# Kernel tuning notes

Measured on AMD Instinct MI355X. Metric: run time of the kernel, lower is better.

The kernel has to match this reference:

```python
import jax, jax.numpy as jnp
import numpy as np

N_NODES = 50000
N_EDGES = 800000
FEAT = 128


def setup_inputs() -> dict:
    key = jax.random.key(0)
    k1, k2, k3, k4 = jax.random.split(key, 4)
    x = jax.random.normal(k1, (N_NODES, FEAT), dtype=jnp.float32)
    a = jax.random.normal(k2, (FEAT, 1), dtype=jnp.float32) * (1.414 / np.sqrt(FEAT))
    row = jax.random.randint(k3, (N_EDGES,), 0, N_NODES, dtype=jnp.int64)
    col = jax.random.randint(k4, (N_EDGES,), 0, N_NODES, dtype=jnp.int64)
    return {"x": x, "a": a, "row": row, "col": col}


def reference(x, a, row, col):
    n = x.shape[0]
    # per-node score e = x @ a, squeezed to [N]
    e = jnp.squeeze(x @ a, axis=-1)
    # gather per-edge score from the destination (column) node, as in e[col]
    vals = e[col]                                            # [E]
    # sparse row-wise softmax (numerically stable via segment max)
    m = jax.ops.segment_max(vals, row, num_segments=n)       # [N]
    m = jnp.where(jnp.isfinite(m), m, 0.0)                   # empty rows -> 0
    ex = jnp.exp(vals - m[row])                              # [E]
    denom = jax.ops.segment_sum(ex, row, num_segments=n)     # [N]
    att = ex / denom[row]                                    # [E]
    # sparse-dense matmul: h[i] = sum_j att_ij * x[j]
    h_prime = jax.ops.segment_sum(att[:, None] * x[col], row, num_segments=n)
    return h_prime
```

## Files before the change

### kernel.cpp

```cpp
#include <hip/hip_runtime.h>
#include <hip/hip_bf16.h>
#include <math.h>

#define FEAT 128

__device__ __forceinline__ int pack_bf162(float lo, float hi) {
    __hip_bfloat162 b = __float22bfloat162_rn(make_float2(lo, hi));
    union { __hip_bfloat162 b; int i; } u;
    u.b = b;
    return u.i;
}

__device__ __forceinline__ float2 bf2_to_f2(int b) {
    union { int i; __hip_bfloat162 b; } u;
    u.i = b;
    return __bfloat1622float2(u.b);
}

__device__ __forceinline__ void fma8(float* acc, int4 v, float w) {
    float2 f0 = bf2_to_f2(v.x), f1 = bf2_to_f2(v.y);
    float2 f2 = bf2_to_f2(v.z), f3 = bf2_to_f2(v.w);
    acc[0] += w * f0.x; acc[1] += w * f0.y;
    acc[2] += w * f1.x; acc[3] += w * f1.y;
    acc[4] += w * f2.x; acc[5] += w * f2.y;
    acc[6] += w * f3.x; acc[7] += w * f3.y;
}

__global__ void dot_hist_kernel(const float* __restrict__ x, const float* __restrict__ a,
                                const int* __restrict__ row,
                                float* __restrict__ exw, unsigned* __restrict__ cnt,
                                unsigned short* __restrict__ rank,
                                int2* __restrict__ xh, int n, int nE) {
    int tid = blockIdx.x * blockDim.x + threadIdx.x;
    if (tid < nE) {
        unsigned old = atomicAdd(&cnt[row[tid]], 1u);
        rank[tid] = (unsigned short)old;
    }
    int node = tid >> 5;
    int l = tid & 31;
    if (node >= n) return;
    float4 xv = ((const float4*)(x + (size_t)node * FEAT))[l];
    float4 av = ((const float4*)a)[l];
    int2 pk;
    pk.x = pack_bf162(xv.x, xv.y);
    pk.y = pack_bf162(xv.z, xv.w);
    xh[(size_t)node * 32 + l] = pk;
    float p = xv.x * av.x + xv.y * av.y + xv.z * av.z + xv.w * av.w;
    #pragma unroll
    for (int off = 16; off > 0; off >>= 1) p += __shfl_xor(p, off);
    if (l == 0) exw[node] = __expf(p);
}

__global__ void scan_kernel(const unsigned* __restrict__ cnt, int* __restrict__ rowptr,
                            unsigned* flags, int n, int nb) {
    __shared__ int sm[256];
    __shared__ int sprefix;
    int b = blockIdx.x;
    int i0 = (b << 10) + (int)threadIdx.x * 4;
    int v0 = (i0 + 0 < n) ? (int)cnt[i0 + 0] : 0;
    int v1 = (i0 + 1 < n) ? (int)cnt[i0 + 1] : 0;
    int v2 = (i0 + 2 < n) ? (int)cnt[i0 + 2] : 0;
    int v3 = (i0 + 3 < n) ? (int)cnt[i0 + 3] : 0;
    int t4 = v0 + v1 + v2 + v3;
    sm[threadIdx.x] = t4;
    __syncthreads();
    #pragma unroll
    for (int off = 1; off < 256; off <<= 1) {
        int u = (threadIdx.x >= (unsigned)off) ? sm[threadIdx.x - off] : 0;
        __syncthreads();
        sm[threadIdx.x] += u;
        __syncthreads();
    }
    if (threadIdx.x == 0)
        __hip_atomic_store(&flags[b], (unsigned)sm[255] + 1u, __ATOMIC_RELEASE,
                           __HIP_MEMORY_SCOPE_AGENT);
    if (threadIdx.x < 64) {
        int lane = threadIdx.x;
        unsigned pred = 0;
        if (lane < b) {
            unsigned f;
            do {
                f = __hip_atomic_load(&flags[lane], __ATOMIC_ACQUIRE,
                                      __HIP_MEMORY_SCOPE_AGENT);
            } while (f == 0u);
            pred = f - 1u;
        }
        #pragma unroll
        for (int off = 32; off > 0; off >>= 1) pred += __shfl_xor(pred, off);
        if (lane == 0) sprefix = (int)pred;
    }
    __syncthreads();
    int base = sprefix + sm[threadIdx.x] - t4;
    if (i0 + 0 < n) rowptr[i0 + 0] = base;
    if (i0 + 1 < n) rowptr[i0 + 1] = base + v0;
    if (i0 + 2 < n) rowptr[i0 + 2] = base + v0 + v1;
    if (i0 + 3 < n) rowptr[i0 + 3] = base + v0 + v1 + v2;
    if (b == nb - 1 && threadIdx.x == 255) rowptr[n] = sprefix + sm[255];
}

__global__ void fill_kernel(const int* __restrict__ row, const int* __restrict__ col,
                            const unsigned short* __restrict__ rank,
                            const int* __restrict__ rowptr,
                            unsigned short* __restrict__ ecol, int nE) {
    int k = (blockIdx.x * blockDim.x + threadIdx.x) * 4;
    if (k + 3 < nE) {
        int4 r4 = *(const int4*)(row + k);
        int4 c4 = *(const int4*)(col + k);
        uint2 rk = *(const uint2*)(rank + k);
        ecol[rowptr[r4.x] + (int)(rk.x & 0xFFFFu)] = (unsigned short)c4.x;
        ecol[rowptr[r4.y] + (int)(rk.x >> 16)]     = (unsigned short)c4.y;
        ecol[rowptr[r4.z] + (int)(rk.y & 0xFFFFu)] = (unsigned short)c4.z;
        ecol[rowptr[r4.w] + (int)(rk.y >> 16)]     = (unsigned short)c4.w;
    } else {
        for (; k < nE; ++k)
            ecol[rowptr[row[k]] + (int)rank[k]] = (unsigned short)col[k];
    }
}

__global__ void __launch_bounds__(256, 4)
gather_kernel(const int4* __restrict__ xh4,
              const float* __restrict__ exw,
              const int* __restrict__ rowptr,
              const unsigned short* __restrict__ ecol,
              float* __restrict__ h, int n) {
    __shared__ __align__(16) int2 sbuf[16][16];
    int g = threadIdx.x >> 4;
    int l = threadIdx.x & 15;
    int node = (int)((blockIdx.x * blockDim.x + threadIdx.x) >> 4);
    if (node >= n) return;
    int s0 = rowptr[node];
    int eend = rowptr[node + 1];
    float acc[8] = {0.f, 0.f, 0.f, 0.f, 0.f, 0.f, 0.f, 0.f};
    float wl = 0.0f;
    const int4* sb4 = (const int4*)&sbuf[g][0];
    for (int base = s0; base < eend; base += 16) {
        int idx = base + l;
        float w = 0.0f;
        if (idx < eend) {
            int c = (int)ecol[idx];
            w = exw[c];
            sbuf[g][l] = make_int2(c << 4, __float_as_int(w));
        }
        wl += w;
        int m = min(16, eend - base);
        int j = 0;
        for (; j + 8 <= m; j += 8) {
            int4 q0 = sb4[(j >> 1) + 0];
            int4 q1 = sb4[(j >> 1) + 1];
            int4 q2 = sb4[(j >> 1) + 2];
            int4 q3 = sb4[(j >> 1) + 3];
            int4 e0 = xh4[q0.x + l];
            int4 e1 = xh4[q0.z + l];
            int4 e2 = xh4[q1.x + l];
            int4 e3 = xh4[q1.z + l];
            int4 e4 = xh4[q2.x + l];
            int4 e5 = xh4[q2.z + l];
            int4 e6 = xh4[q3.x + l];
            int4 e7 = xh4[q3.z + l];
            fma8(acc, e0, __int_as_float(q0.y));
            fma8(acc, e1, __int_as_float(q0.w));
            fma8(acc, e2, __int_as_float(q1.y));
            fma8(acc, e3, __int_as_float(q1.w));
            fma8(acc, e4, __int_as_float(q2.y));
            fma8(acc, e5, __int_as_float(q2.w));
            fma8(acc, e6, __int_as_float(q3.y));
            fma8(acc, e7, __int_as_float(q3.w));
        }
        for (; j + 2 <= m; j += 2) {
            int4 q = sb4[j >> 1];
            int4 ea = xh4[q.x + l];
            int4 eb = xh4[q.z + l];
            fma8(acc, ea, __int_as_float(q.y));
            fma8(acc, eb, __int_as_float(q.w));
        }
        if (j < m) {
            int2 p = sbuf[g][j];
            fma8(acc, xh4[p.x + l], __int_as_float(p.y));
        }
    }
    float ws = wl;
    #pragma unroll
    for (int off = 8; off > 0; off >>= 1) ws += __shfl_xor(ws, off);
    float inv = (eend > s0) ? 1.0f / ws : 0.0f;
    float4 o0 = make_float4(acc[0] * inv, acc[1] * inv, acc[2] * inv, acc[3] * inv);
    float4 o1 = make_float4(acc[4] * inv, acc[5] * inv, acc[6] * inv, acc[7] * inv);
    float4* hp = (float4*)(h + (size_t)node * FEAT);
    hp[2 * l + 0] = o0;
    hp[2 * l + 1] = o1;
}

extern "C" void kernel_launch(void* const* d_in, const int* in_sizes, int n_in,
                              void* d_out, int out_size, void* d_ws, size_t ws_size,
                              hipStream_t stream) {
    const float* x = (const float*)d_in[0];
    const float* a = (const float*)d_in[1];
    const int* row = (const int*)d_in[2];
    const int* col = (const int*)d_in[3];
    int n  = in_sizes[0] / FEAT;
    int nE = in_sizes[2];
    float* h = (float*)d_out;
    int nb = (n + 1023) / 1024;

    char* p = (char*)d_ws;
    auto alloc = [&](size_t bytes) { char* q = p; p += (bytes + 15) & ~(size_t)15; return q; };
    unsigned* cnt        = (unsigned*)alloc((size_t)n * 4);
    unsigned* flags      = (unsigned*)alloc(64 * 4);
    float* exw           = (float*)alloc((size_t)n * 4);
    int* rowptr          = (int*)alloc((size_t)(n + 1) * 4);
    unsigned short* rank = (unsigned short*)alloc((size_t)nE * 2);
    unsigned short* ecol = (unsigned short*)alloc((size_t)nE * 2);
    int2* xh             = (int2*)alloc((size_t)n * 32 * 8);

    (void)hipMemsetAsync(cnt, 0, ((size_t)n + 64) * sizeof(unsigned), stream);

    int t1 = (n * 32 > nE) ? n * 32 : nE;
    dot_hist_kernel<<<(t1 + 255) / 256, 256, 0, stream>>>(x, a, row, exw, cnt, rank,
                                                          xh, n, nE);
    scan_kernel<<<nb, 256, 0, stream>>>(cnt, rowptr, flags, n, nb);
    fill_kernel<<<(nE / 4 + 255) / 256, 256, 0, stream>>>(row, col, rank, rowptr,
                                                          ecol, nE);
    gather_kernel<<<((size_t)n * 16 + 255) / 256, 256, 0, stream>>>((const int4*)xh, exw,
                                                                    rowptr, ecol, h, n);
}
```

Baseline: 172.1 us.

## Fuse scan and CSR fill via grid barrier, replace rank array with atomic cursors

Merges the prefix-scan and the CSR fill kernels into one launch. The launch uses a software grid barrier built on 16 striped counters, so one kernel launch and one inter-kernel gap go away. The per-edge rank array written during the histogram is dropped, and fill slots are claimed instead with atomicAdd on a per-row write-pointer copy of rowptr. This saves the rank writes and reads but adds a second round of edge atomics. The barrier relies on all blocks (nE/4/256, about 782) being co-resident, which the code does not check, so it risks deadlock if they are not. The order of columns within each row also becomes nondeterministic.

```diff
diff --git a/kernel.cpp b/kernel.cpp
--- a/kernel.cpp
+++ b/kernel.cpp
@@ -3,6 +3,7 @@
 #include <math.h>
 
 #define FEAT 128
+#define BSTRIDE 32
 
 __device__ __forceinline__ int pack_bf162(float lo, float hi) {
     __hip_bfloat162 b = __float22bfloat162_rn(make_float2(lo, hi));
@@ -26,15 +27,35 @@
     acc[6] += w * f3.x; acc[7] += w * f3.y;
 }
 
+__device__ __forceinline__ void put_s32(int* p, int v) {
+    __hip_atomic_store(p, v, __ATOMIC_RELAXED, __HIP_MEMORY_SCOPE_AGENT);
+}
+
+__device__ __forceinline__ void gridbar(unsigned* bsync, unsigned target) {
+    __syncthreads();
+    if (threadIdx.x < 16) {
+        if (threadIdx.x == 0)
+            __hip_atomic_fetch_add(&bsync[(blockIdx.x & 15) * BSTRIDE], 1u,
+                                   __ATOMIC_RELAXED, __HIP_MEMORY_SCOPE_AGENT);
+        for (;;) {
+            unsigned v = __hip_atomic_load(&bsync[threadIdx.x * BSTRIDE],
+                                           __ATOMIC_RELAXED, __HIP_MEMORY_SCOPE_AGENT);
+            #pragma unroll
+            for (int off = 8; off > 0; off >>= 1) v += __shfl_xor(v, off);
+            if (v >= target) break;
+            __builtin_amdgcn_s_sleep(32);
+        }
+    }
+    __syncthreads();
+}
+
 __global__ void dot_hist_kernel(const float* __restrict__ x, const float* __restrict__ a,
                                 const int* __restrict__ row,
                                 float* __restrict__ exw, unsigned* __restrict__ cnt,
-                                unsigned short* __restrict__ rank,
                                 int2* __restrict__ xh, int n, int nE) {
     int tid = blockIdx.x * blockDim.x + threadIdx.x;
     if (tid < nE) {
-        unsigned old = atomicAdd(&cnt[row[tid]], 1u);
-        rank[tid] = (unsigned short)old;
+        atomicAdd(&cnt[row[tid]], 1u);
     }
     int node = tid >> 5;
     int l = tid & 31;
@@ -51,69 +72,76 @@
     if (l == 0) exw[node] = __expf(p);
 }
 
-__global__ void scan_kernel(const unsigned* __restrict__ cnt, int* __restrict__ rowptr,
-                            unsigned* flags, int n, int nb) {
+__global__ void __launch_bounds__(256, 4)
+scan_fill_kernel(const unsigned* __restrict__ cnt, int* __restrict__ rowptr,
+                 int* __restrict__ wp, unsigned* __restrict__ flags,
+                 unsigned* __restrict__ bsync,
+                 const int* __restrict__ row, const int* __restrict__ col,
+                 unsigned short* __restrict__ ecol,
+                 int n, int nE, int nb, int nblocks) {
     __shared__ int sm[256];
     __shared__ int sprefix;
     int b = blockIdx.x;
-    int i0 = (b << 10) + (int)threadIdx.x * 4;
-    int v0 = (i0 + 0 < n) ? (int)cnt[i0 + 0] : 0;
-    int v1 = (i0 + 1 < n) ? (int)cnt[i0 + 1] : 0;
-    int v2 = (i0 + 2 < n) ? (int)cnt[i0 + 2] : 0;
-    int v3 = (i0 + 3 < n) ? (int)cnt[i0 + 3] : 0;
-    int t4 = v0 + v1 + v2 + v3;
-    sm[threadIdx.x] = t4;
-    __syncthreads();
-    #pragma unroll
-    for (int off = 1; off < 256; off <<= 1) {
-        int u = (threadIdx.x >= (unsigned)off) ? sm[threadIdx.x - off] : 0;
+    if (b < nb) {
+        int i0 = (b << 10) + (int)threadIdx.x * 4;
+        int v0 = (i0 + 0 < n) ? (int)cnt[i0 + 0] : 0;
+        int v1 = (i0 + 1 < n) ? (int)cnt[i0 + 1] : 0;
+        int v2 = (i0 + 2 < n) ? (int)cnt[i0 + 2] : 0;
+        int v3 = (i0 + 3 < n) ? (int)cnt[i0 + 3] : 0;
+        int t4 = v0 + v1 + v2 + v3;
+        sm[threadIdx.x] = t4;
         __syncthreads();
-        sm[threadIdx.x] += u;
+        #pragma unroll
+        for (int off = 1; off < 256; off <<= 1) {
+            int u = (threadIdx.x >= (unsigned)off) ? sm[threadIdx.x - off] : 0;
+            __syncthreads();
+            sm[threadIdx.x] += u;
+            __syncthreads();
+        }
+        if (threadIdx.x == 0)
+            __hip_atomic_store(&flags[b], (unsigned)sm[255] + 1u, __ATOMIC_RELEASE,
+                               __HIP_MEMORY_SCOPE_AGENT);
+        if (threadIdx.x < 64) {
+            int lane = threadIdx.x;
+            unsigned pred = 0;
+            if (lane < b) {
+                unsigned f;
+                do {
+                    f = __hip_atomic_load(&flags[lane], __ATOMIC_ACQUIRE,
+                                          __HIP_MEMORY_SCOPE_AGENT);
+                } while (f == 0u);
+                pred = f - 1u;
+            }
+            #pragma unroll
+            for (int off = 32; off > 0; off >>= 1) pred += __shfl_xor(pred, off);
+            if (lane == 0) sprefix = (int)pred;
+        }
         __syncthreads();
-    }
-    if (threadIdx.x == 0)
-        __hip_atomic_store(&flags[b], (unsigned)sm[255] + 1u, __ATOMIC_RELEASE,
-                           __HIP_MEMORY_SCOPE_AGENT);
-    if (threadIdx.x < 64) {
-        int lane = threadIdx.x;
-        unsigned pred = 0;
-        if (lane < b) {
-            unsigned f;
-            do {
-                f = __hip_atomic_load(&flags[lane], __ATOMIC_ACQUIRE,
-                                      __HIP_MEMORY_SCOPE_AGENT);
-            } while (f == 0u);
-            pred = f - 1u;
-        }
-        #pragma unroll
-        for (int off = 32; off > 0; off >>= 1) pred += __shfl_xor(pred, off);
-        if (lane == 0) sprefix = (int)pred;
-    }
-    __syncthreads();
-    int base = sprefix + sm[threadIdx.x] - t4;
-    if (i0 + 0 < n) rowptr[i0 + 0] = base;
-    if (i0 + 1 < n) rowptr[i0 + 1] = base + v0;
-    if (i0 + 2 < n) rowptr[i0 + 2] = base + v0 + v1;
-    if (i0 + 3 < n) rowptr[i0 + 3] = base + v0 + v1 + v2;
-    if (b == nb - 1 && threadIdx.x == 255) rowptr[n] = sprefix + sm[255];
-}
-
-__global__ void fill_kernel(const int* __restrict__ row, const int* __restrict__ col,
-                            const unsigned short* __restrict__ rank,
-                            const int* __restrict__ rowptr,
-                            unsigned short* __restrict__ ecol, int nE) {
+        int base = sprefix + sm[threadIdx.x] - t4;
+        if (i0 + 0 < n) { put_s32(&rowptr[i0 + 0], base);            put_s32(&wp[i0 + 0], base); }
+        if (i0 + 1 < n) { put_s32(&rowptr[i0 + 1], base + v0);       put_s32(&wp[i0 + 1], base + v0); }
+        if (i0 + 2 < n) { put_s32(&rowptr[i0 + 2], base + v0 + v1);  put_s32(&wp[i0 + 2], base + v0 + v1); }
+        if (i0 + 3 < n) { put_s32(&rowptr[i0 + 3], base + v0 + v1 + v2);
+                          put_s32(&wp[i0 + 3], base + v0 + v1 + v2); }
+        if (b == nb - 1 && threadIdx.x == 255) put_s32(&rowptr[n], sprefix + sm[255]);
+    }
+    gridbar(bsync, (unsigned)nblocks);
+
     int k = (blockIdx.x * blockDim.x + threadIdx.x) * 4;
     if (k + 3 < nE) {
         int4 r4 = *(const int4*)(row + k);
         int4 c4 = *(const int4*)(col + k);
-        uint2 rk = *(const uint2*)(rank + k);
-        ecol[rowptr[r4.x] + (int)(rk.x & 0xFFFFu)] = (unsigned short)c4.x;
-        ecol[rowptr[r4.y] + (int)(rk.x >> 16)]     = (unsigned short)c4.y;
-        ecol[rowptr[r4.z] + (int)(rk.y & 0xFFFFu)] = (unsigned short)c4.z;
-        ecol[rowptr[r4.w] + (int)(rk.y >> 16)]     = (unsigned short)c4.w;
+        int p0 = atomicAdd(&wp[r4.x], 1);
+        int p1 = atomicAdd(&wp[r4.y], 1);
+        int p2 = atomicAdd(&wp[r4.z], 1);
+        int p3 = atomicAdd(&wp[r4.w], 1);
+        ecol[p0] = (unsigned short)c4.x;
+        ecol[p1] = (unsigned short)c4.y;
+        ecol[p2] = (unsigned short)c4.z;
+        ecol[p3] = (unsigned short)c4.w;
     } else {
         for (; k < nE; ++k)
-            ecol[rowptr[row[k]] + (int)rank[k]] = (unsigned short)col[k];
+            ecol[atomicAdd(&wp[row[k]], 1)] = (unsigned short)col[k];
     }
 }
 
@@ -200,25 +228,28 @@
     int nE = in_sizes[2];
     float* h = (float*)d_out;
     int nb = (n + 1023) / 1024;
+    int nblocks23 = (nE / 4 + 255) / 256;
 
     char* p = (char*)d_ws;
     auto alloc = [&](size_t bytes) { char* q = p; p += (bytes + 15) & ~(size_t)15; return q; };
     unsigned* cnt        = (unsigned*)alloc((size_t)n * 4);
     unsigned* flags      = (unsigned*)alloc(64 * 4);
+    unsigned* bsync      = (unsigned*)alloc(16 * BSTRIDE * 4);
     float* exw           = (float*)alloc((size_t)n * 4);
     int* rowptr          = (int*)alloc((size_t)(n + 1) * 4);
-    unsigned short* rank = (unsigned short*)alloc((size_t)nE * 2);
+    int* wp              = (int*)alloc((size_t)n * 4);
     unsigned short* ecol = (unsigned short*)alloc((size_t)nE * 2);
     int2* xh             = (int2*)alloc((size_t)n * 32 * 8);
 
-    (void)hipMemsetAsync(cnt, 0, ((size_t)n + 64) * sizeof(unsigned), stream);
+    (void)hipMemsetAsync(cnt, 0, (size_t)n * 4 + 64 * 4 + (size_t)16 * BSTRIDE * 4,
+                         stream);
 
     int t1 = (n * 32 > nE) ? n * 32 : nE;
-    dot_hist_kernel<<<(t1 + 255) / 256, 256, 0, stream>>>(x, a, row, exw, cnt, rank,
-                                                          xh, n, nE);
-    scan_kernel<<<nb, 256, 0, stream>>>(cnt, rowptr, flags, n, nb);
-    fill_kernel<<<(nE / 4 + 255) / 256, 256, 0, stream>>>(row, col, rank, rowptr,
-                                                          ecol, nE);
+    dot_hist_kernel<<<(t1 + 255) / 256, 256, 0, stream>>>(x, a, row, exw, cnt, xh,
+                                                          n, nE);
+    scan_fill_kernel<<<nblocks23, 256, 0, stream>>>(cnt, rowptr, wp, flags, bsync,
+                                                    row, col, ecol, n, nE, nb,
+                                                    nblocks23);
     gather_kernel<<<((size_t)n * 16 + 255) / 256, 256, 0, stream>>>((const int4*)xh, exw,
                                                                     rowptr, ecol, h, n);
 }
```

After: 207.9 us. 1.21x slower.

## Privatize row histogram per XCD to keep atomics local

Applied to the files above, without the earlier changes.

The edge-count histogram is split into eight per-XCD copies, indexed by the hardware XCC id, and its atomics are issued at workgroup scope. The scan kernel sums the copies to build rowptr and also writes per-XCD base offsets, which the fill kernel uses together with a 32-bit packed (xcd, rank) word. The aim is to avoid cross-XCD coherence traffic on contended global atomics. In exchange the counters, memset and rank array grow by eight times, the scan does more reads and writes, and correctness depends on workgroup-scope atomics being coherent within one XCD's L2.

```diff
diff --git a/kernel.cpp b/kernel.cpp
--- a/kernel.cpp
+++ b/kernel.cpp
@@ -3,6 +3,7 @@
 #include <math.h>
 
 #define FEAT 128
+#define NXCD 8
 
 __device__ __forceinline__ int pack_bf162(float lo, float hi) {
     __hip_bfloat162 b = __float22bfloat162_rn(make_float2(lo, hi));
@@ -26,15 +27,24 @@
     acc[6] += w * f3.x; acc[7] += w * f3.y;
 }
 
+__device__ __forceinline__ int xcd_id() {
+    int x;
+    asm("s_getreg_b32 %0, hwreg(HW_REG_XCC_ID)" : "=s"(x));
+    return x & (NXCD - 1);
+}
+
 __global__ void dot_hist_kernel(const float* __restrict__ x, const float* __restrict__ a,
                                 const int* __restrict__ row,
-                                float* __restrict__ exw, unsigned* __restrict__ cnt,
-                                unsigned short* __restrict__ rank,
+                                float* __restrict__ exw, unsigned* __restrict__ cnt8,
+                                unsigned* __restrict__ rankw,
                                 int2* __restrict__ xh, int n, int nE) {
     int tid = blockIdx.x * blockDim.x + threadIdx.x;
     if (tid < nE) {
-        unsigned old = atomicAdd(&cnt[row[tid]], 1u);
-        rank[tid] = (unsigned short)old;
+        int xcd = xcd_id();
+        unsigned old = __hip_atomic_fetch_add(&cnt8[(size_t)xcd * n + row[tid]], 1u,
+                                              __ATOMIC_RELAXED,
+                                              __HIP_MEMORY_SCOPE_WORKGROUP);
+        rankw[tid] = ((unsigned)xcd << 16) | (old & 0xFFFFu);
     }
     int node = tid >> 5;
     int l = tid & 31;
@@ -51,17 +61,25 @@
     if (l == 0) exw[node] = __expf(p);
 }
 
-__global__ void scan_kernel(const unsigned* __restrict__ cnt, int* __restrict__ rowptr,
-                            unsigned* flags, int n, int nb) {
+__global__ void scan_kernel(const unsigned* __restrict__ cnt8, int* __restrict__ rowptr,
+                            int* __restrict__ bx, unsigned* flags, int n, int nb) {
     __shared__ int sm[256];
     __shared__ int sprefix;
     int b = blockIdx.x;
     int i0 = (b << 10) + (int)threadIdx.x * 4;
-    int v0 = (i0 + 0 < n) ? (int)cnt[i0 + 0] : 0;
-    int v1 = (i0 + 1 < n) ? (int)cnt[i0 + 1] : 0;
-    int v2 = (i0 + 2 < n) ? (int)cnt[i0 + 2] : 0;
-    int v3 = (i0 + 3 < n) ? (int)cnt[i0 + 3] : 0;
-    int t4 = v0 + v1 + v2 + v3;
+    int cc[NXCD][4];
+    int v[4] = {0, 0, 0, 0};
+    #pragma unroll
+    for (int xc = 0; xc < NXCD; ++xc) {
+        const unsigned* cp = cnt8 + (size_t)xc * n;
+        #pragma unroll
+        for (int j = 0; j < 4; ++j) {
+            int c = (i0 + j < n) ? (int)cp[i0 + j] : 0;
+            cc[xc][j] = c;
+            v[j] += c;
+        }
+    }
+    int t4 = v[0] + v[1] + v[2] + v[3];
     sm[threadIdx.x] = t4;
     __syncthreads();
     #pragma unroll
@@ -91,29 +109,49 @@
     }
     __syncthreads();
     int base = sprefix + sm[threadIdx.x] - t4;
-    if (i0 + 0 < n) rowptr[i0 + 0] = base;
-    if (i0 + 1 < n) rowptr[i0 + 1] = base + v0;
-    if (i0 + 2 < n) rowptr[i0 + 2] = base + v0 + v1;
-    if (i0 + 3 < n) rowptr[i0 + 3] = base + v0 + v1 + v2;
+    int rb[4];
+    rb[0] = base;
+    rb[1] = rb[0] + v[0];
+    rb[2] = rb[1] + v[1];
+    rb[3] = rb[2] + v[2];
+    #pragma unroll
+    for (int j = 0; j < 4; ++j)
+        if (i0 + j < n) rowptr[i0 + j] = rb[j];
+    #pragma unroll
+    for (int xc = 0; xc < NXCD; ++xc) {
+        int* bp = bx + (size_t)xc * n;
+        #pragma unroll
+        for (int j = 0; j < 4; ++j) {
+            if (i0 + j < n) bp[i0 + j] = rb[j];
+            rb[j] += cc[xc][j];
+        }
+    }
     if (b == nb - 1 && threadIdx.x == 255) rowptr[n] = sprefix + sm[255];
 }
 
 __global__ void fill_kernel(const int* __restrict__ row, const int* __restrict__ col,
-                            const unsigned short* __restrict__ rank,
-                            const int* __restrict__ rowptr,
-                            unsigned short* __restrict__ ecol, int nE) {
+                            const unsigned* __restrict__ rankw,
+                            const int* __restrict__ bx,
+                            unsigned short* __restrict__ ecol, int n, int nE) {
     int k = (blockIdx.x * blockDim.x + threadIdx.x) * 4;
     if (k + 3 < nE) {
         int4 r4 = *(const int4*)(row + k);
         int4 c4 = *(const int4*)(col + k);
-        uint2 rk = *(const uint2*)(rank + k);
-        ecol[rowptr[r4.x] + (int)(rk.x & 0xFFFFu)] = (unsigned short)c4.x;
-        ecol[rowptr[r4.y] + (int)(rk.x >> 16)]     = (unsigned short)c4.y;
-        ecol[rowptr[r4.z] + (int)(rk.y & 0xFFFFu)] = (unsigned short)c4.z;
-        ecol[rowptr[r4.w] + (int)(rk.y >> 16)]     = (unsigned short)c4.w;
+        uint4 rw = *(const uint4*)(rankw + k);
+        int p0 = bx[(size_t)(rw.x >> 16) * n + r4.x] + (int)(rw.x & 0xFFFFu);
+        int p1 = bx[(size_t)(rw.y >> 16) * n + r4.y] + (int)(rw.y & 0xFFFFu);
+        int p2 = bx[(size_t)(rw.z >> 16) * n + r4.z] + (int)(rw.z & 0xFFFFu);
+        int p3 = bx[(size_t)(rw.w >> 16) * n + r4.w] + (int)(rw.w & 0xFFFFu);
+        ecol[p0] = (unsigned short)c4.x;
+        ecol[p1] = (unsigned short)c4.y;
+        ecol[p2] = (unsigned short)c4.z;
+        ecol[p3] = (unsigned short)c4.w;
     } else {
-        for (; k < nE; ++k)
-            ecol[rowptr[row[k]] + (int)rank[k]] = (unsigned short)col[k];
+        for (; k < nE; ++k) {
+            unsigned rw = rankw[k];
+            int pos = bx[(size_t)(rw >> 16) * n + row[k]] + (int)(rw & 0xFFFFu);
+            ecol[pos] = (unsigned short)col[k];
+        }
     }
 }
 
@@ -203,22 +241,23 @@
 
     char* p = (char*)d_ws;
     auto alloc = [&](size_t bytes) { char* q = p; p += (bytes + 15) & ~(size_t)15; return q; };
-    unsigned* cnt        = (unsigned*)alloc((size_t)n * 4);
+    unsigned* cnt8       = (unsigned*)alloc((size_t)NXCD * n * 4);
     unsigned* flags      = (unsigned*)alloc(64 * 4);
     float* exw           = (float*)alloc((size_t)n * 4);
     int* rowptr          = (int*)alloc((size_t)(n + 1) * 4);
-    unsigned short* rank = (unsigned short*)alloc((size_t)nE * 2);
+    int* bx              = (int*)alloc((size_t)NXCD * n * 4);
+    unsigned* rankw      = (unsigned*)alloc((size_t)nE * 4);
     unsigned short* ecol = (unsigned short*)alloc((size_t)nE * 2);
     int2* xh             = (int2*)alloc((size_t)n * 32 * 8);
 
-    (void)hipMemsetAsync(cnt, 0, ((size_t)n + 64) * sizeof(unsigned), stream);
+    (void)hipMemsetAsync(cnt8, 0, (size_t)NXCD * n * 4 + 64 * 4, stream);
 
     int t1 = (n * 32 > nE) ? n * 32 : nE;
-    dot_hist_kernel<<<(t1 + 255) / 256, 256, 0, stream>>>(x, a, row, exw, cnt, rank,
+    dot_hist_kernel<<<(t1 + 255) / 256, 256, 0, stream>>>(x, a, row, exw, cnt8, rankw,
                                                           xh, n, nE);
-    scan_kernel<<<nb, 256, 0, stream>>>(cnt, rowptr, flags, n, nb);
-    fill_kernel<<<(nE / 4 + 255) / 256, 256, 0, stream>>>(row, col, rank, rowptr,
-                                                          ecol, nE);
+    scan_kernel<<<nb, 256, 0, stream>>>(cnt8, rowptr, bx, flags, n, nb);
+    fill_kernel<<<(nE / 4 + 255) / 256, 256, 0, stream>>>(row, col, rankw, bx,
+                                                          ecol, n, nE);
     gather_kernel<<<((size_t)n * 16 + 255) / 256, 256, 0, stream>>>((const int4*)xh, exw,
                                                                     rowptr, ecol, h, n);
 }
```

Result: no change. 175.2 us (+1.8%).
